# Kernel tuning notes

Hardware: AMD Instinct MI355X
Metric: run time of the kernel (lower is better)

Reference implementation:

```python
import jax, jax.numpy as jnp
import numpy as np

B, C, H, W = 4, 16, 512, 512

# 8-connectivity offsets in the exact order the torch double loop visits them
_OFFSETS = [(-1, -1), (-1, 0), (-1, 1), (0, -1), (0, 1), (1, -1), (1, 0), (1, 1)]


def _make_edge_index(height, width):
    """Vectorized grid_8 edge index, matching torch's per-node-then-offset order."""
    n = height * width
    dst = np.zeros((n, 8), dtype=np.int64)
    mask = np.zeros((n, 8), dtype=bool)
    hh = np.arange(height)[:, None]
    ww = np.arange(width)[None, :]
    for k, (dh, dw) in enumerate(_OFFSETS):
        nh, nw = hh + dh, ww + dw
        valid = (nh >= 0) & (nh < height) & (nw >= 0) & (nw < width)
        nb = np.clip(nh, 0, height - 1) * width + np.clip(nw, 0, width - 1)
        dst[:, k] = nb.reshape(-1)
        mask[:, k] = valid.reshape(-1)
    src = np.repeat(np.arange(n, dtype=np.int64), 8).reshape(n, 8)
    m = mask.reshape(-1)
    return np.stack([src.reshape(-1)[m], dst.reshape(-1)[m]], axis=0)  # [2, E]


def setup_inputs() -> dict:
    key = jax.random.key(0)
    grid_features = jax.random.normal(key, (B, C, H, W), dtype=jnp.float32)
    edge_index = jnp.asarray(_make_edge_index(H, W))  # [2, 2091012]
    return {"grid_features": grid_features, "edge_index": edge_index}


def reference(grid_features, edge_index):
    b, c, h, w = grid_features.shape
    # (B, C, H, W) -> (B*H*W, C) node features
    grid_flat = jnp.transpose(grid_features, (0, 2, 3, 1)).reshape(b, h * w, c)
    node_features = grid_flat.reshape(b * h * w, c)

    src, dst = edge_index[0], edge_index[1]
    src_h, src_w = src // w, src % w
    dst_h, dst_w = dst // w, dst % w
    spatial_dist = jnp.sqrt(
        (src_h - dst_h).astype(jnp.float32) ** 2
        + (src_w - dst_w).astype(jnp.float32) ** 2
    )  # [E]

    # per-edge |src - dst| feature diff, mean over channels, then mean over batch
    diff = jnp.abs(grid_flat[:, src, :] - grid_flat[:, dst, :]).mean(axis=-1)  # [B, E]
    feature_diff = diff.mean(axis=0)  # [E]

    edge_attr = jnp.stack([spatial_dist, feature_diff], axis=1)  # [E, 2]
    return node_features, edge_index, edge_attr
```

## Files before the change

### kernel.cpp

```cpp
#include <hip/hip_runtime.h>

#define HW  (512 * 512)
#define NC  16
#define NB  4
#define GW  512
#define GH  512
#define TILE 16
#define HALO 18
#define NSU  12
#define NDS_U (HALO * HALO * NSU)

typedef _Float16 h2 __attribute__((ext_vector_type(2)));
typedef __fp16  h2raw __attribute__((ext_vector_type(2)));

__device__ __forceinline__ unsigned int pk16(float a, float b) {
    h2raw h = __builtin_amdgcn_cvt_pkrtz(a, b);
    return __builtin_bit_cast(unsigned int, h);
}
__device__ __forceinline__ h2 asH(unsigned int u) {
    return __builtin_bit_cast(h2, u);
}
__device__ __forceinline__ float flo(unsigned int u) { return (float)asH(u).x; }
__device__ __forceinline__ float fhi(unsigned int u) { return (float)asH(u).y; }
__device__ __forceinline__ h2 absdiff(h2 x, h2 y) {
    h2 d = x - y;
    unsigned int u = __builtin_bit_cast(unsigned int, d) & 0x7fff7fffu;
    return __builtin_bit_cast(h2, u);
}

__device__ __forceinline__ int edge_prefix(int h, int w) {
    if (h == 0) return (w == 0) ? 0 : 3 + 5 * (w - 1);
    int p = 2556 + 4090 * (h - 1);
    if (h == GH - 1) return p + ((w == 0) ? 0 : 3 + 5 * (w - 1));
    return p + ((w == 0) ? 0 : 5 + 8 * (w - 1));
}
__device__ __forceinline__ int degree(int h, int w) {
    int rh = 1 + (h > 0) + (h < GH - 1);
    int rw = 1 + (w > 0) + (w < GW - 1);
    return rh * rw - 1;
}

#define STAGE_LOAD(bb)                                                         \
    do {                                                                       \
        _Pragma("unroll") for (int r = 0; r < 4; ++r) if (vld[r]) {            \
            const float* p = g + (size_t)off0[r] + ((size_t)(bb) << 22);       \
            LA[r] = *(const float4*)p;                                         \
            LB[r] = *(const float4*)(p + HW);                                  \
        }                                                                      \
    } while (0)

#define STAGE_WRITE(buf)                                                       \
    do {                                                                       \
        _Pragma("unroll") for (int r = 0; r < 4; ++r) if (vld[r]) {            \
            _Pragma("unroll") for (int j = 0; j < 4; ++j) {                    \
                int hc = vhc[r] + j;                                           \
                if ((unsigned)hc < (unsigned)HALO)                             \
                    (buf)[vslot[r] + j * NSU] =                                \
                        pk16(((const float*)&LA[r])[j], ((const float*)&LB[r])[j]); \
            }                                                                  \
        }                                                                      \
    } while (0)

__global__ __launch_bounds__(256) void k_fused(const float* __restrict__ g,
                                               float* __restrict__ nf_out,
                                               float* __restrict__ ei_out,
                                               float* __restrict__ attr_out,
                                               int E) {
    __shared__ unsigned int nds[2][NDS_U];
    float* fdbuf = (float*)nds;

    const int tid = threadIdx.x;
    const int xk = blockIdx.x & 7;
    const int m  = blockIdx.x >> 3;
    const int by = ((xk >> 2) << 4) | (m >> 3);
    const int bx = ((xk & 3) << 3) | (m & 7);
    const int h0 = by * TILE, w0 = bx * TILE;
    const int tr = tid >> 4, tc = tid & 15;

    const int OFF_H[8] = {-1, -1, -1, 0, 0, 1, 1, 1};
    const int OFF_W[8] = {-1, 0, 1, -1, 1, -1, 0, 1};

    bool vld[4];
    int off0[4], vslot[4], vhc[4];
#pragma unroll
    for (int r = 0; r < 4; ++r) {
        int idx = r * 256 + tid;
        vld[r] = idx < 864;
        int i2  = vld[r] ? idx : 0;
        int f4  = i2 % 6;
        int t   = i2 / 6;
        int row = t % 18;
        int c2  = t / 18;
        int hh  = min(max(h0 - 1 + row, 0), GH - 1);
        int gw  = min(max(w0 - 4 + 4 * f4, 0), GW - 4);
        off0[r]  = ((2 * c2) << 18) + (hh << 9) + gw;
        vhc[r]   = 4 * f4 - 3;
        vslot[r] = (row * HALO + vhc[r]) * NSU + c2;
    }

    float acc[8];
#pragma unroll
    for (int k = 0; k < 8; ++k) acc[k] = 0.0f;

    float4 LA[4], LB[4];
    STAGE_LOAD(0);

#pragma unroll 1
    for (int b = 0; b < NB; ++b) {
        unsigned int* buf = nds[b & 1];

        STAGE_WRITE(buf);
        __syncthreads();

        if (b + 1 < NB) STAGE_LOAD(b + 1);

#pragma unroll
        for (int s = 0; s < 4; ++s) {
            int o4 = s * 256 + tid;
            int c4 = o4 & 3;
            int nl256 = o4 >> 2;
            int pr = nl256 >> 4, pc = nl256 & 15;
            int nl = (pr + 1) * HALO + (pc + 1);
            unsigned int u0 = buf[nl * NSU + 2 * c4];
            unsigned int u1 = buf[nl * NSU + 2 * c4 + 1];
            int n = (h0 + pr) * GW + (w0 + pc);
            float4* dst = (float4*)(nf_out + (((size_t)b << 18) + n) * NC + 4 * c4);
            *dst = make_float4(flo(u0), fhi(u0), flo(u1), fhi(u1));
        }

        {
            const uint4* p = (const uint4*)buf;
            int nl_self = (tr + 1) * HALO + (tc + 1);
            uint4 s0 = p[nl_self * 3];
            uint4 s1 = p[nl_self * 3 + 1];
            h2 sf[8] = { asH(s0.x), asH(s0.y), asH(s0.z), asH(s0.w),
                         asH(s1.x), asH(s1.y), asH(s1.z), asH(s1.w) };
#pragma unroll
            for (int k = 0; k < 8; ++k) {
                int nl_n = (tr + 1 + OFF_H[k]) * HALO + (tc + 1 + OFF_W[k]);
                uint4 n0 = p[nl_n * 3];
                uint4 n1 = p[nl_n * 3 + 1];
                h2 a0 = absdiff(sf[0], asH(n0.x));
                h2 a1 = absdiff(sf[1], asH(n0.y));
                h2 a2 = absdiff(sf[2], asH(n0.z));
                h2 a3 = absdiff(sf[3], asH(n0.w));
                h2 a4 = absdiff(sf[4], asH(n1.x));
                h2 a5 = absdiff(sf[5], asH(n1.y));
                h2 a6 = absdiff(sf[6], asH(n1.z));
                h2 a7 = absdiff(sf[7], asH(n1.w));
                h2 b0 = a0 + a1, b1 = a2 + a3, b2 = a4 + a5, b3 = a6 + a7;
                h2 c0 = b0 + b1, c1 = b2 + b3;
                acc[k] += ((float)c0.x + (float)c0.y) + ((float)c1.x + (float)c1.y);
            }
        }
    }

    __syncthreads();

    {
        int h = h0 + tr, w = w0 + tc;
        int cnt = 0;
#pragma unroll
        for (int k = 0; k < 8; ++k) {
            if ((unsigned)(h + OFF_H[k]) < (unsigned)GH &&
                (unsigned)(w + OFF_W[k]) < (unsigned)GW) {
                fdbuf[tid * 9 + cnt] = acc[k] * (1.0f / 64.0f);
                ++cnt;
            }
        }
    }
    __syncthreads();

#pragma unroll
    for (int r = 0; r < 8; ++r) {
        int u2    = r * 256 + tid;
        int chunk = u2 >> 7;
        int e     = u2 & 127;
        int h     = h0 + chunk;
        int first = degree(h, w0);
        int mid   = degree(h, w0 + 1);
        int last  = degree(h, w0 + TILE - 1);
        int Lr    = first + 14 * mid + last;
        if (e < Lr) {
            int node_in_row, k;
            if (e < first) { node_in_row = 0; k = e; }
            else {
                int m2 = e - first;
                if (mid == 8) { node_in_row = 1 + (m2 >> 3); k = m2 & 7; }
                else          { int q = m2 / 5; node_in_row = 1 + q; k = m2 - 5 * q; }
            }
            int w = w0 + node_in_row;
            int n = h * GW + w;
            int idx = 0, cnt2 = 0;
#pragma unroll
            for (int i = 0; i < 8; ++i) {
                bool ok = (unsigned)(h + OFF_H[i]) < (unsigned)GH &&
                          (unsigned)(w + OFF_W[i]) < (unsigned)GW;
                if (ok) { if (cnt2 == k) idx = i; ++cnt2; }
            }
            int dh = OFF_H[idx], dw = OFF_W[idx];
            float dist = (dh != 0 && dw != 0) ? 1.41421356237f : 1.0f;
            float fd = fdbuf[(chunk * 16 + node_in_row) * 9 + k];
            int o = edge_prefix(h, w0) + e;
            ei_out[o]     = (float)n;
            ei_out[E + o] = (float)(n + dh * GW + dw);
            *(float2*)(attr_out + 2 * (size_t)o) = make_float2(dist, fd);
        }
    }
}

extern "C" void kernel_launch(void* const* d_in, const int* in_sizes, int n_in,
                              void* d_out, int out_size, void* d_ws, size_t ws_size,
                              hipStream_t stream) {
    const float* g = (const float*)d_in[0];
    int E = in_sizes[1] / 2;

    float* out      = (float*)d_out;
    float* nf_out   = out;
    float* ei_out   = out + (size_t)NB * HW * NC;
    float* attr_out = ei_out + (size_t)2 * E;

    k_fused<<<(GH / TILE) * (GW / TILE), 256, 0, stream>>>(g, nf_out, ei_out, attr_out, E);
}
```

Measured before the change: 175.4 us.

## Give each wavefront a private quadrant halo to drop block barriers

The 16x16 tile is split into four 8x8 quadrants, one per wavefront. Each wavefront stages its own 10x10 halo into a private LDS region for every batch. The per-batch __syncthreads is replaced by a wave-local lgkmcnt wait, so waves no longer stall on each other during the batch loop. The cost is about a quarter more global halo loads (overlapping quadrant borders) and a larger LDS footprint, which could lower occupancy.

```diff
diff --git a/kernel.cpp b/kernel.cpp
--- a/kernel.cpp
+++ b/kernel.cpp
@@ -6,9 +6,9 @@
 #define GW  512
 #define GH  512
 #define TILE 16
-#define HALO 18
+#define QHALO 10
 #define NSU  12
-#define NDS_U (HALO * HALO * NSU)
+#define WREG (QHALO * QHALO * NSU)
 
 typedef _Float16 h2 __attribute__((ext_vector_type(2)));
 typedef __fp16  h2raw __attribute__((ext_vector_type(2)));
@@ -42,20 +42,20 @@
 
 #define STAGE_LOAD(bb)                                                         \
     do {                                                                       \
-        _Pragma("unroll") for (int r = 0; r < 4; ++r) if (vld[r]) {            \
+        _Pragma("unroll") for (int r = 0; r < 5; ++r) {                        \
             const float* p = g + (size_t)off0[r] + ((size_t)(bb) << 22);       \
             LA[r] = *(const float4*)p;                                         \
             LB[r] = *(const float4*)(p + HW);                                  \
         }                                                                      \
     } while (0)
 
-#define STAGE_WRITE(buf)                                                       \
+#define STAGE_WRITE(wbuf)                                                      \
     do {                                                                       \
-        _Pragma("unroll") for (int r = 0; r < 4; ++r) if (vld[r]) {            \
+        _Pragma("unroll") for (int r = 0; r < 5; ++r) {                        \
             _Pragma("unroll") for (int j = 0; j < 4; ++j) {                    \
                 int hc = vhc[r] + j;                                           \
-                if ((unsigned)hc < (unsigned)HALO)                             \
-                    (buf)[vslot[r] + j * NSU] =                                \
+                if ((unsigned)hc < (unsigned)QHALO)                            \
+                    (wbuf)[vslot[r] + j * NSU] =                               \
                         pk16(((const float*)&LA[r])[j], ((const float*)&LB[r])[j]); \
             }                                                                  \
         }                                                                      \
@@ -66,78 +66,80 @@
                                                float* __restrict__ ei_out,
                                                float* __restrict__ attr_out,
                                                int E) {
-    __shared__ unsigned int nds[2][NDS_U];
+    __shared__ unsigned int nds[2][4][WREG];
     float* fdbuf = (float*)nds;
 
-    const int tid = threadIdx.x;
+    const int tid  = threadIdx.x;
+    const int wv   = tid >> 6;
+    const int lane = tid & 63;
+    const int qr = wv >> 1, qc = wv & 1;
+
     const int xk = blockIdx.x & 7;
     const int m  = blockIdx.x >> 3;
     const int by = ((xk >> 2) << 4) | (m >> 3);
     const int bx = ((xk & 3) << 3) | (m & 7);
     const int h0 = by * TILE, w0 = bx * TILE;
-    const int tr = tid >> 4, tc = tid & 15;
+    const int h0q = h0 + 8 * qr, w0q = w0 + 8 * qc;
 
     const int OFF_H[8] = {-1, -1, -1, 0, 0, 1, 1, 1};
     const int OFF_W[8] = {-1, 0, 1, -1, 1, -1, 0, 1};
 
-    bool vld[4];
-    int off0[4], vslot[4], vhc[4];
-#pragma unroll
-    for (int r = 0; r < 4; ++r) {
-        int idx = r * 256 + tid;
-        vld[r] = idx < 864;
-        int i2  = vld[r] ? idx : 0;
-        int f4  = i2 % 6;
-        int t   = i2 / 6;
-        int row = t % 18;
-        int c2  = t / 18;
-        int hh  = min(max(h0 - 1 + row, 0), GH - 1);
-        int gw  = min(max(w0 - 4 + 4 * f4, 0), GW - 4);
+    int off0[5], vslot[5], vhc[5];
+#pragma unroll
+    for (int r = 0; r < 5; ++r) {
+        int s   = r * 64 + lane;
+        int f4  = s & 3;
+        int t   = s >> 2;
+        int row = t % 10;
+        int c2  = t / 10;
+        int hh  = min(max(h0q - 1 + row, 0), GH - 1);
+        int gw  = min(max(w0q - 4 + 4 * f4, 0), GW - 4);
         off0[r]  = ((2 * c2) << 18) + (hh << 9) + gw;
         vhc[r]   = 4 * f4 - 3;
-        vslot[r] = (row * HALO + vhc[r]) * NSU + c2;
+        vslot[r] = (row * QHALO + vhc[r]) * NSU + c2;
     }
 
     float acc[8];
 #pragma unroll
     for (int k = 0; k < 8; ++k) acc[k] = 0.0f;
 
-    float4 LA[4], LB[4];
+    float4 LA[5], LB[5];
     STAGE_LOAD(0);
 
 #pragma unroll 1
     for (int b = 0; b < NB; ++b) {
-        unsigned int* buf = nds[b & 1];
-
-        STAGE_WRITE(buf);
-        __syncthreads();
+        unsigned int* wbuf = nds[b & 1][wv];
+
+        STAGE_WRITE(wbuf);
+        asm volatile("s_waitcnt lgkmcnt(0)" ::: "memory");
 
         if (b + 1 < NB) STAGE_LOAD(b + 1);
 
 #pragma unroll
         for (int s = 0; s < 4; ++s) {
-            int o4 = s * 256 + tid;
+            int o4 = s * 64 + lane;
             int c4 = o4 & 3;
-            int nl256 = o4 >> 2;
-            int pr = nl256 >> 4, pc = nl256 & 15;
-            int nl = (pr + 1) * HALO + (pc + 1);
-            unsigned int u0 = buf[nl * NSU + 2 * c4];
-            unsigned int u1 = buf[nl * NSU + 2 * c4 + 1];
-            int n = (h0 + pr) * GW + (w0 + pc);
+            int nd = o4 >> 2;
+            int pr = nd >> 3, pc = nd & 7;
+            int nl = (pr + 1) * QHALO + (pc + 1);
+            unsigned int u0 = wbuf[nl * NSU + 2 * c4];
+            unsigned int u1 = wbuf[nl * NSU + 2 * c4 + 1];
+            int n = (h0q + pr) * GW + (w0q + pc);
             float4* dst = (float4*)(nf_out + (((size_t)b << 18) + n) * NC + 4 * c4);
             *dst = make_float4(flo(u0), fhi(u0), flo(u1), fhi(u1));
         }
 
         {
-            const uint4* p = (const uint4*)buf;
-            int nl_self = (tr + 1) * HALO + (tc + 1);
+            const uint4* p = (const uint4*)wbuf;
+            int pr = lane >> 3, pc = lane & 7;
+            int nl_self = (pr + 1) * QHALO + (pc + 1);
             uint4 s0 = p[nl_self * 3];
             uint4 s1 = p[nl_self * 3 + 1];
             h2 sf[8] = { asH(s0.x), asH(s0.y), asH(s0.z), asH(s0.w),
                          asH(s1.x), asH(s1.y), asH(s1.z), asH(s1.w) };
 #pragma unroll
             for (int k = 0; k < 8; ++k) {
-                int nl_n = (tr + 1 + OFF_H[k]) * HALO + (tc + 1 + OFF_W[k]);
+                int nl_n = (pr + 1 + OFF_H[k]) * QHALO + (pc + 1 + OFF_W[k]);
                 uint4 n0 = p[nl_n * 3];
                 uint4 n1 = p[nl_n * 3 + 1];
                 h2 a0 = absdiff(sf[0], asH(n0.x));
@@ -158,13 +160,15 @@
     __syncthreads();
 
     {
-        int h = h0 + tr, w = w0 + tc;
+        int pr = lane >> 3, pc = lane & 7;
+        int h = h0q + pr, w = w0q + pc;
+        int tn = (8 * qr + pr) * 16 + (8 * qc + pc);
         int cnt = 0;
 #pragma unroll
         for (int k = 0; k < 8; ++k) {
             if ((unsigned)(h + OFF_H[k]) < (unsigned)GH &&
                 (unsigned)(w + OFF_W[k]) < (unsigned)GW) {
-                fdbuf[tid * 9 + cnt] = acc[k] * (1.0f / 64.0f);
+                fdbuf[tn * 9 + cnt] = acc[k] * (1.0f / 64.0f);
                 ++cnt;
             }
         }
```

Measured after the change: 184.3 us. 5.1% more time.
